# Performance work log

Hardware: AMD Instinct MI355X
Metric: run time of the kernel (lower is better)

## Reference

```python
import jax, jax.numpy as jnp
import numpy as np

def setup_inputs() -> dict:
    key = jax.random.key(0)
    inputs_embeds = jax.random.normal(key, (16, 8192, 256), dtype=jnp.float32)
    return {"inputs_embeds": inputs_embeds}

def reference(inputs_embeds):
    # cumulative prefix mean along seq dim: mean over [:i+1] = cumsum / (i+1)
    S = inputs_embeds.shape[1]
    csum = jnp.cumsum(inputs_embeds, axis=1)  # [B, S, D]
    denom = jnp.arange(1, S + 1, dtype=inputs_embeds.dtype)[None, :, None]
    return (csum / denom,)
```

## Files before the change

kernel.cpp:

```cpp
#include <hip/hip_runtime.h>

#define BB 16
#define SS 8192
#define DD 256
#define D4 (DD / 4)
#define NC 256
#define CL (SS / NC)
#define G  16

__global__ __launch_bounds__(64) void avgseq_chunksum(const float4* __restrict__ x,
                                                      float4* __restrict__ ws) {
    const int blk = blockIdx.x;
    const int b = blk >> 8;
    const int c = blk & (NC - 1);
    const int t = threadIdx.x;

    const float4* p = x + ((size_t)b * SS + (size_t)c * CL) * D4 + t;
    float4 acc = make_float4(0.f, 0.f, 0.f, 0.f);
    for (int s0 = 0; s0 < CL; s0 += G) {
        float4 v[G];
#pragma unroll
        for (int g = 0; g < G; ++g) v[g] = p[(size_t)(s0 + g) * D4];
#pragma unroll
        for (int g = 0; g < G; ++g) {
            acc.x += v[g].x; acc.y += v[g].y; acc.z += v[g].z; acc.w += v[g].w;
        }
    }
    ws[((size_t)b * NC + c) * D4 + t] = acc;
}

__global__ __launch_bounds__(64) void avgseq_scanws(float4* __restrict__ ws) {
    const int b = blockIdx.x;
    const int t = threadIdx.x;
    float4* w = ws + (size_t)b * NC * D4 + t;
    float4 run = make_float4(0.f, 0.f, 0.f, 0.f);
#pragma unroll 8
    for (int c = 0; c < NC; ++c) {
        float4 v = w[(size_t)c * D4];
        w[(size_t)c * D4] = run;
        run.x += v.x; run.y += v.y; run.z += v.z; run.w += v.w;
    }
}

__global__ __launch_bounds__(64) void avgseq_scan(const float4* __restrict__ x,
                                                  const float4* __restrict__ ws,
                                                  float4* __restrict__ out) {
    const int blk = blockIdx.x;
    const int b = blk >> 8;
    const int c = blk & (NC - 1);
    const int t = threadIdx.x;

    float4 acc = ws[((size_t)b * NC + c) * D4 + t];

    const size_t base = ((size_t)b * SS + (size_t)c * CL) * D4 + t;
    const float4* p = x + base;
    float4* o = out + base;
    const int s0 = c * CL;

    for (int ss = 0; ss < CL; ss += G) {
        float4 v[G];
#pragma unroll
        for (int g = 0; g < G; ++g) v[g] = p[(size_t)(ss + g) * D4];
        float4 ov[G];
#pragma unroll
        for (int g = 0; g < G; ++g) {
            acc.x += v[g].x; acc.y += v[g].y; acc.z += v[g].z; acc.w += v[g].w;
            const float r = __builtin_amdgcn_rcpf((float)(s0 + ss + g + 1));
            ov[g] = make_float4(acc.x * r, acc.y * r, acc.z * r, acc.w * r);
        }
#pragma unroll
        for (int g = 0; g < G; ++g) o[(size_t)(ss + g) * D4] = ov[g];
    }
}

extern "C" void kernel_launch(void* const* d_in, const int* in_sizes, int n_in,
                              void* d_out, int out_size, void* d_ws, size_t ws_size,
                              hipStream_t stream) {
    const float4* x = (const float4*)d_in[0];
    float4* out = (float4*)d_out;
    float4* ws = (float4*)d_ws;

    const int nblocks = BB * NC;
    avgseq_chunksum<<<nblocks, 64, 0, stream>>>(x, ws);
    avgseq_scanws<<<BB, 64, 0, stream>>>(ws);
    avgseq_scan<<<nblocks, 64, 0, stream>>>(x, ws, out);
}
```

Before: 260.9 us.

## Replace three-kernel chunked scan with single-pass decoupled lookback scan

Merges the chunk-sum, workspace-scan and output-scan kernels into one kernel that uses decoupled lookback. Each block publishes its local aggregate and then its inclusive prefix through flags in the workspace, while successor blocks spin on those flags. This removes a kernel launch and the serial workspace scan. It also adds nontemporal output stores. The input chunk is still read twice, and correctness relies on blocks being scheduled in order and on enough workspace; otherwise the old path runs.

```diff
diff --git a/kernel.cpp b/kernel.cpp
--- a/kernel.cpp
+++ b/kernel.cpp
@@ -8,13 +8,118 @@
 #define CL (SS / NC)
 #define G  16
 
+#define NBLK (BB * NC)
+#define AGGA_OFF (64 * 1024)
+#define AGG_BYTES (NBLK * DD * 4)
+#define AGGI_OFF (AGGA_OFF + AGG_BYTES)
+#define WS_NEEDED ((size_t)(AGGI_OFF + AGG_BYTES))
+
+typedef float nat4 __attribute__((ext_vector_type(4)));
+
+union F2U { float2 f; unsigned long long u; };
+
+__global__ __launch_bounds__(256) void avgseq_init(int* __restrict__ flags) {
+    const int i = blockIdx.x * 256 + threadIdx.x;
+    if (i < NBLK) flags[i] = 0;
+}
+
+__global__ __launch_bounds__(64, 4) void avgseq_lookback(
+    const float4* __restrict__ x, float4* __restrict__ out,
+    int* __restrict__ flags, unsigned long long* __restrict__ aggA,
+    unsigned long long* __restrict__ aggI)
+{
+    const int blk = blockIdx.x;
+    const int b = blk >> 8;
+    const int c = blk & (NC - 1);
+    const int t = threadIdx.x;
+
+    const size_t base = ((size_t)b * SS + (size_t)c * CL) * D4 + t;
+    const float4* p = x + base;
+
+    float4 agg = make_float4(0.f, 0.f, 0.f, 0.f);
+    for (int s0 = 0; s0 < CL; s0 += G) {
+        float4 v[G];
+#pragma unroll
+        for (int g = 0; g < G; ++g) v[g] = p[(size_t)(s0 + g) * D4];
+#pragma unroll
+        for (int g = 0; g < G; ++g) {
+            agg.x += v[g].x; agg.y += v[g].y; agg.z += v[g].z; agg.w += v[g].w;
+        }
+    }
+
+    const size_t slot = (size_t)blk * (DD / 2) + (size_t)t * 2;
+
+    if (c > 0) {
+        F2U lo, hi;
+        lo.f = make_float2(agg.x, agg.y);
+        hi.f = make_float2(agg.z, agg.w);
+        __hip_atomic_store(&aggA[slot],     lo.u, __ATOMIC_RELAXED, __HIP_MEMORY_SCOPE_AGENT);
+        __hip_atomic_store(&aggA[slot + 1], hi.u, __ATOMIC_RELAXED, __HIP_MEMORY_SCOPE_AGENT);
+        asm volatile("s_waitcnt vmcnt(0)" ::: "memory");
+        __hip_atomic_store(&flags[blk], 1, __ATOMIC_RELAXED, __HIP_MEMORY_SCOPE_AGENT);
+    }
+
+    double rx = 0.0, ry = 0.0, rz = 0.0, rw = 0.0;
+    if (c > 0) {
+        int cc = c - 1;
+        for (;;) {
+            const int fblk = (b << 8) + cc;
+            int f;
+            for (;;) {
+                f = __hip_atomic_load(&flags[fblk], __ATOMIC_RELAXED, __HIP_MEMORY_SCOPE_AGENT);
+                f = __builtin_amdgcn_readfirstlane(f);
+                if (f != 0) break;
+                __builtin_amdgcn_s_sleep(1);
+            }
+            const unsigned long long* src = (f == 2) ? aggI : aggA;
+            const size_t s2 = (size_t)fblk * (DD / 2) + (size_t)t * 2;
+            F2U a, bq;
+            a.u  = __hip_atomic_load(&src[s2],     __ATOMIC_RELAXED, __HIP_MEMORY_SCOPE_AGENT);
+            bq.u = __hip_atomic_load(&src[s2 + 1], __ATOMIC_RELAXED, __HIP_MEMORY_SCOPE_AGENT);
+            rx += a.f.x; ry += a.f.y; rz += bq.f.x; rw += bq.f.y;
+            if (f == 2) break;
+            --cc;
+        }
+    }
+    const float4 run = make_float4((float)rx, (float)ry, (float)rz, (float)rw);
+
+    if (c < NC - 1) {
+        F2U lo, hi;
+        lo.f = make_float2(run.x + agg.x, run.y + agg.y);
+        hi.f = make_float2(run.z + agg.z, run.w + agg.w);
+        __hip_atomic_store(&aggI[slot],     lo.u, __ATOMIC_RELAXED, __HIP_MEMORY_SCOPE_AGENT);
+        __hip_atomic_store(&aggI[slot + 1], hi.u, __ATOMIC_RELAXED, __HIP_MEMORY_SCOPE_AGENT);
+        asm volatile("s_waitcnt vmcnt(0)" ::: "memory");
+        __hip_atomic_store(&flags[blk], 2, __ATOMIC_RELAXED, __HIP_MEMORY_SCOPE_AGENT);
+    }
+
+    float4 acc = run;
+    float4* o = out + base;
+    const int sb = c * CL;
+    for (int s0 = 0; s0 < CL; s0 += G) {
+        float4 v[G];
+#pragma unroll
+        for (int g = 0; g < G; ++g) v[g] = p[(size_t)(s0 + g) * D4];
+#pragma unroll
+        for (int g = 0; g < G; ++g) {
+            acc.x += v[g].x; acc.y += v[g].y; acc.z += v[g].z; acc.w += v[g].w;
+            const float r = __builtin_amdgcn_rcpf((float)(sb + s0 + g + 1));
+            v[g] = make_float4(acc.x * r, acc.y * r, acc.z * r, acc.w * r);
+        }
+#pragma unroll
+        for (int g = 0; g < G; ++g) {
+            nat4 nv = { v[g].x, v[g].y, v[g].z, v[g].w };
+            __builtin_nontemporal_store(nv, (nat4*)&o[(size_t)(s0 + g) * D4]);
+        }
+    }
+}
+
 __global__ __launch_bounds__(64) void avgseq_chunksum(const float4* __restrict__ x,
                                                       float4* __restrict__ ws) {
     const int blk = blockIdx.x;
     const int b = blk >> 8;
     const int c = blk & (NC - 1);
     const int t = threadIdx.x;
-
     const float4* p = x + ((size_t)b * SS + (size_t)c * CL) * D4 + t;
     float4 acc = make_float4(0.f, 0.f, 0.f, 0.f);
     for (int s0 = 0; s0 < CL; s0 += G) {
@@ -49,27 +154,23 @@
     const int b = blk >> 8;
     const int c = blk & (NC - 1);
     const int t = threadIdx.x;
-
     float4 acc = ws[((size_t)b * NC + c) * D4 + t];
-
     const size_t base = ((size_t)b * SS + (size_t)c * CL) * D4 + t;
     const float4* p = x + base;
     float4* o = out + base;
     const int s0 = c * CL;
-
     for (int ss = 0; ss < CL; ss += G) {
         float4 v[G];
 #pragma unroll
         for (int g = 0; g < G; ++g) v[g] = p[(size_t)(ss + g) * D4];
-        float4 ov[G];
 #pragma unroll
         for (int g = 0; g < G; ++g) {
             acc.x += v[g].x; acc.y += v[g].y; acc.z += v[g].z; acc.w += v[g].w;
             const float r = __builtin_amdgcn_rcpf((float)(s0 + ss + g + 1));
-            ov[g] = make_float4(acc.x * r, acc.y * r, acc.z * r, acc.w * r);
+            v[g] = make_float4(acc.x * r, acc.y * r, acc.z * r, acc.w * r);
         }
 #pragma unroll
-        for (int g = 0; g < G; ++g) o[(size_t)(ss + g) * D4] = ov[g];
+        for (int g = 0; g < G; ++g) o[(size_t)(ss + g) * D4] = v[g];
     }
 }
 
@@ -78,10 +179,17 @@
                               hipStream_t stream) {
     const float4* x = (const float4*)d_in[0];
     float4* out = (float4*)d_out;
-    float4* ws = (float4*)d_ws;
 
-    const int nblocks = BB * NC;
-    avgseq_chunksum<<<nblocks, 64, 0, stream>>>(x, ws);
-    avgseq_scanws<<<BB, 64, 0, stream>>>(ws);
-    avgseq_scan<<<nblocks, 64, 0, stream>>>(x, ws, out);
+    if (ws_size >= WS_NEEDED) {
+        int* flags = (int*)d_ws;
+        unsigned long long* aggA = (unsigned long long*)((char*)d_ws + AGGA_OFF);
+        unsigned long long* aggI = (unsigned long long*)((char*)d_ws + AGGI_OFF);
+        avgseq_init<<<(NBLK + 255) / 256, 256, 0, stream>>>(flags);
+        avgseq_lookback<<<NBLK, 64, 0, stream>>>(x, out, flags, aggA, aggI);
+    } else {
+        float4* ws = (float4*)d_ws;
+        avgseq_chunksum<<<NBLK, 64, 0, stream>>>(x, ws);
+        avgseq_scanws<<<BB, 64, 0, stream>>>(ws);
+        avgseq_scan<<<NBLK, 64, 0, stream>>>(x, ws, out);
+    }
 }
```

Result: slower. 272.1 us (+4.3%).
